# Kernel tuning notes

Measured on AMD Instinct MI355X. Metric: run time of the kernel, lower is better.

The kernel has to match this reference:

```python
import jax, jax.numpy as jnp
import numpy as np

B, S, IDIM, D, T, DUR_MAX = 32, 512, 256, 256, 4096, 16
EPS = 1e-6
SIGMA_C = 2.0
PAD = 0
LOG_SQRT_2PI = 0.9189385332046727  # 0.5*log(2*pi)


def setup_inputs() -> dict:
    rng = np.random.default_rng(0)
    # durations in [1, DUR_MAX); clip so each row's total length <= T (ragged tails)
    durs = rng.integers(1, DUR_MAX, size=(B, S))
    excl = np.cumsum(durs, axis=-1) - durs
    durs = np.minimum(durs, np.maximum(T - excl, 0))
    # token ids in [1, IDIM) so PAD=0 only appears via explicit padding
    text = rng.integers(1, IDIM, size=(B, S))
    embed = rng.standard_normal((IDIM, D)).astype(np.float32)
    embed[PAD] = 0.0  # padding_idx=0 row is zeros in nn.Embedding
    return {
        "text": jnp.asarray(text, dtype=jnp.int64),
        "durs": jnp.asarray(durs, dtype=jnp.int64),
        "embed": jnp.asarray(embed),
        "total_time": T,
    }


def reference(text, durs, embed, total_time):
    # F.pad(text/durs, [0, 2]) with value 0
    text_p = jnp.pad(text, ((0, 0), (0, 2)), constant_values=PAD)   # [B, S+2]
    durs_p = jnp.pad(durs, ((0, 0), (0, 2)), constant_values=0)     # [B, S+2]
    S2 = text_p.shape[-1]

    cum = jnp.cumsum(durs_p, axis=-1)                               # [B, S+2]
    durs_f = durs_p.astype(jnp.float32)
    # token centers: durs/2 + exclusive cumsum
    c = durs_f / 2.0 + (cum - durs_p).astype(jnp.float32)           # [B, S+2]
    sig = durs_f / SIGMA_C + EPS                                    # [B, S+2]

    t = jnp.arange(total_time, dtype=jnp.float32) + 0.5             # [T]
    z = (t[None, :, None] - c[:, None, :]) / sig[:, None, :]        # [B, T, S+2]
    # Normal(c, sig).log_prob(t).exp()
    w = jnp.exp(-0.5 * z * z - jnp.log(sig)[:, None, :] - LOG_SQRT_2PI)

    # zero weights on pad tokens, then normalize over tokens
    token_pad = (text_p == PAD)                                     # [B, S+2]
    w = jnp.where(token_pad[:, None, :], 0.0, w)
    w = w / (w.sum(-1, keepdims=True) + EPS)

    # frames beyond a row's total duration correspond to pad in `repeats`:
    # zero all weights there, then set the last token column to 1.0
    time_invalid = jnp.arange(total_time)[None, :] >= cum[:, -1:]   # [B, T]
    w = jnp.where(time_invalid[:, :, None], 0.0, w)
    last_col = (jnp.arange(S2) == S2 - 1)
    w = jnp.where(time_invalid[:, :, None] & last_col[None, None, :], 1.0, w)

    emb = embed[text_p]                                             # [B, S+2, D]
    return jnp.einsum("bts,bsd->btd", w, emb)                       # [B, T, D]
```

## Files before the change

kernel.cpp:

```cpp
#include <hip/hip_runtime.h>

#define B_ 32
#define S_ 512
#define D_ 256
#define T_ 4096
#define IDIM_ 256
#define EPS_ 1e-6f
#define INV_SQRT_2PI 0.3989422804014327f
#define NHALF_LOG2E -0.7213475204444817f
#define W_ 48

__global__ __launch_bounds__(512) void GaussianEmbedding_prep(
    const int* __restrict__ text, const int* __restrict__ durs,
    float4* __restrict__ toks, int* __restrict__ tof, int* __restrict__ totb)
{
    int b = blockIdx.x;
    int s = threadIdx.x;
    int dur = durs[b * S_ + s];
    int lane = s & 63, wv = s >> 6;

    int incl = dur;
    #pragma unroll
    for (int o = 1; o < 64; o <<= 1) {
        int v = __shfl_up(incl, o);
        if (lane >= o) incl += v;
    }
    __shared__ int wsum[8];
    if (lane == 63) wsum[wv] = incl;
    __syncthreads();
    int woff = 0;
    for (int i = 0; i < wv; ++i) woff += wsum[i];
    int excl = woff + incl - dur;

    if (s == 0) {
        int tot = 0;
        for (int i = 0; i < 8; ++i) tot += wsum[i];
        totb[b] = tot;
    }

    float df = (float)dur;
    float sig = df * 0.5f + EPS_;
    float inv = 1.0f / sig;
    float4 tk;
    tk.x = df * 0.5f + (float)excl;
    tk.y = inv;
    tk.z = INV_SQRT_2PI * inv;
    tk.w = __int_as_float(text[b * S_ + s] & (IDIM_ - 1));
    toks[b * S_ + s] = tk;

    for (int f = excl; f < excl + dur; ++f)
        tof[b * T_ + f] = s;
}

__global__ __launch_bounds__(256) void GaussianEmbedding_main(
    const float4* __restrict__ toks, const int* __restrict__ tof,
    const int* __restrict__ totb, const float* __restrict__ embed,
    float4* __restrict__ out)
{
    int wv = threadIdx.x >> 6;
    int lane = threadIdx.x & 63;
    int frame = __builtin_amdgcn_readfirstlane(blockIdx.x * 4 + wv);
    int b = frame >> 12;
    int t = frame & (T_ - 1);

    int total = totb[b];
    float4 acc = make_float4(0.f, 0.f, 0.f, 0.f);

    if (t < total) {
        int tlo = t - W_; if (tlo < 0) tlo = 0;
        int thi = t + W_; if (thi > total - 1) thi = total - 1;
        int lo = tof[b * T_ + tlo];
        int hi = tof[b * T_ + thi];

        float tc = (float)t + 0.5f;
        float psum = 0.f;
        for (int s = lo; s <= hi; ++s) {
            float4 tk = toks[b * S_ + s];
            float z = (tc - tk.x) * tk.y;
            float w = exp2f(NHALF_LOG2E * z * z) * tk.z;
            psum += w;
            int tok = __float_as_int(tk.w);
            float4 ev = ((const float4*)embed)[tok * (D_ / 4) + lane];
            acc.x += w * ev.x;
            acc.y += w * ev.y;
            acc.z += w * ev.z;
            acc.w += w * ev.w;
        }
        float invp = 1.0f / (psum + EPS_);
        acc.x *= invp; acc.y *= invp; acc.z *= invp; acc.w *= invp;
    }
    out[(size_t)frame * (D_ / 4) + lane] = acc;
}

extern "C" void kernel_launch(void* const* d_in, const int* in_sizes, int n_in,
                              void* d_out, int out_size, void* d_ws, size_t ws_size,
                              hipStream_t stream)
{
    const int* text    = (const int*)d_in[0];
    const int* durs    = (const int*)d_in[1];
    const float* embed = (const float*)d_in[2];

    float4* toks = (float4*)d_ws;
    int* tof  = (int*)((char*)d_ws + (size_t)B_ * S_ * sizeof(float4));
    int* totb = tof + (size_t)B_ * T_;

    GaussianEmbedding_prep<<<B_, S_, 0, stream>>>(text, durs, toks, tof, totb);
    GaussianEmbedding_main<<<(B_ * T_) / 4, 256, 0, stream>>>(
        toks, tof, totb, embed, (float4*)d_out);
}
```

Measured before the change: 183.3 us.

## Stage per-block token window in LDS, shrink window, use nontemporal stores

Each block of 4 frames now computes one shared token range, loads those token records into shared memory once, and has all four waves loop over the staged tokens. The window shrinks from 48 to 32 frames and is capped at 128 tokens. Output is written with nontemporal stores to avoid polluting cache, and the inner loop is unrolled by 4. The shared range is a union over four frames, so each wave evaluates a few extra negligible tokens, and two block-wide barriers are added; the narrower window slightly changes the approximation of the full-sequence normalization.

```diff
diff --git a/kernel.cpp b/kernel.cpp
--- a/kernel.cpp
+++ b/kernel.cpp
@@ -8,7 +8,10 @@
 #define EPS_ 1e-6f
 #define INV_SQRT_2PI 0.3989422804014327f
 #define NHALF_LOG2E -0.7213475204444817f
-#define W_ 48
+#define W_ 32
+#define NMAX_ 128
+
+typedef float float4n __attribute__((ext_vector_type(4)));
 
 __global__ __launch_bounds__(512) void GaussianEmbedding_prep(
     const int* __restrict__ text, const int* __restrict__ durs,
@@ -55,41 +58,61 @@
 __global__ __launch_bounds__(256) void GaussianEmbedding_main(
     const float4* __restrict__ toks, const int* __restrict__ tof,
     const int* __restrict__ totb, const float* __restrict__ embed,
-    float4* __restrict__ out)
+    float* __restrict__ out)
 {
     int wv = threadIdx.x >> 6;
     int lane = threadIdx.x & 63;
-    int frame = __builtin_amdgcn_readfirstlane(blockIdx.x * 4 + wv);
-    int b = frame >> 12;
-    int t = frame & (T_ - 1);
+    int blk = blockIdx.x;
+    int b  = blk >> 10;
+    int t0 = (blk & 1023) * 4;
 
     int total = totb[b];
-    float4 acc = make_float4(0.f, 0.f, 0.f, 0.f);
 
+    __shared__ float4 stoks[NMAX_];
+    __shared__ int shead[2];
+
+    if (threadIdx.x == 0) {
+        int lo = 0, n = 0;
+        if (t0 < total) {
+            int tlo = t0 - W_;      if (tlo < 0) tlo = 0;
+            int thi = t0 + 3 + W_;  if (thi > total - 1) thi = total - 1;
+            lo = tof[b * T_ + tlo];
+            int hi = tof[b * T_ + thi];
+            n = hi - lo + 1;
+            if (n > NMAX_) n = NMAX_;
+        }
+        shead[0] = lo; shead[1] = n;
+    }
+    __syncthreads();
+    int lo = shead[0], n = shead[1];
+    if (threadIdx.x < n)
+        stoks[threadIdx.x] = toks[b * S_ + lo + threadIdx.x];
+    __syncthreads();
+
+    int t = t0 + wv;
+    float4n acc = {0.f, 0.f, 0.f, 0.f};
     if (t < total) {
-        int tlo = t - W_; if (tlo < 0) tlo = 0;
-        int thi = t + W_; if (thi > total - 1) thi = total - 1;
-        int lo = tof[b * T_ + tlo];
-        int hi = tof[b * T_ + thi];
-
         float tc = (float)t + 0.5f;
         float psum = 0.f;
-        for (int s = lo; s <= hi; ++s) {
-            float4 tk = toks[b * S_ + s];
+        const float4* embed4 = (const float4*)embed;
+        #pragma unroll 4
+        for (int i = 0; i < n; ++i) {
+            float4 tk = stoks[i];
             float z = (tc - tk.x) * tk.y;
             float w = exp2f(NHALF_LOG2E * z * z) * tk.z;
             psum += w;
             int tok = __float_as_int(tk.w);
-            float4 ev = ((const float4*)embed)[tok * (D_ / 4) + lane];
+            float4 ev = embed4[tok * (D_ / 4) + lane];
             acc.x += w * ev.x;
             acc.y += w * ev.y;
             acc.z += w * ev.z;
             acc.w += w * ev.w;
         }
         float invp = 1.0f / (psum + EPS_);
-        acc.x *= invp; acc.y *= invp; acc.z *= invp; acc.w *= invp;
+        acc *= invp;
     }
-    out[(size_t)frame * (D_ / 4) + lane] = acc;
+    float4n* outv = (float4n*)out;
+    __builtin_nontemporal_store(acc, &outv[(size_t)(b * T_ + t) * (D_ / 4) + lane]);
 }
 
 extern "C" void kernel_launch(void* const* d_in, const int* in_sizes, int n_in,
@@ -106,5 +129,5 @@
 
     GaussianEmbedding_prep<<<B_, S_, 0, stream>>>(text, durs, toks, tof, totb);
     GaussianEmbedding_main<<<(B_ * T_) / 4, 256, 0, stream>>>(
-        toks, tof, totb, embed, (float4*)d_out);
+        toks, tof, totb, embed, (float*)d_out);
 }
```

Measured after the change: 174.1 us. 1.05x faster.

## Process four frames per wavefront to reuse token and embedding loads

Applied to the files above, without the earlier changes.

Each wavefront now computes four consecutive output frames, so every token record and embedding row it loads is shared across four accumulators instead of being reloaded per frame. The Gaussian window shrinks from 48 to 32 frames, and the prep kernel fills the tail of the frame-to-token map so index lookups past a row's total stay defined. Output is written with nontemporal stores. In exchange there are four times as many accumulator registers, fewer waves in flight, and a truncation window that is narrower and may drop more weight.

```diff
diff --git a/kernel.cpp b/kernel.cpp
--- a/kernel.cpp
+++ b/kernel.cpp
@@ -8,7 +8,9 @@
 #define EPS_ 1e-6f
 #define INV_SQRT_2PI 0.3989422804014327f
 #define NHALF_LOG2E -0.7213475204444817f
-#define W_ 48
+#define W_ 32
+
+typedef float float4n __attribute__((ext_vector_type(4)));
 
 __global__ __launch_bounds__(512) void GaussianEmbedding_prep(
     const int* __restrict__ text, const int* __restrict__ durs,
@@ -26,6 +28,7 @@
         if (lane >= o) incl += v;
     }
     __shared__ int wsum[8];
+    __shared__ int stot;
     if (lane == 63) wsum[wv] = incl;
     __syncthreads();
     int woff = 0;
@@ -36,7 +39,10 @@
         int tot = 0;
         for (int i = 0; i < 8; ++i) tot += wsum[i];
         totb[b] = tot;
+        stot = tot;
     }
+    __syncthreads();
+    int total = stot;
 
     float df = (float)dur;
     float sig = df * 0.5f + EPS_;
@@ -50,46 +56,63 @@
 
     for (int f = excl; f < excl + dur; ++f)
         tof[b * T_ + f] = s;
+    for (int f = total + s; f < T_; f += S_)
+        tof[b * T_ + f] = S_ - 1;
 }
 
 __global__ __launch_bounds__(256) void GaussianEmbedding_main(
-    const float4* __restrict__ toks, const int* __restrict__ tof,
-    const int* __restrict__ totb, const float* __restrict__ embed,
-    float4* __restrict__ out)
+    const float4n* __restrict__ toks, const int* __restrict__ tof,
+    const int* __restrict__ totb, const float4n* __restrict__ embed4,
+    float4n* __restrict__ out)
 {
-    int wv = threadIdx.x >> 6;
     int lane = threadIdx.x & 63;
-    int frame = __builtin_amdgcn_readfirstlane(blockIdx.x * 4 + wv);
-    int b = frame >> 12;
-    int t = frame & (T_ - 1);
+    int wave = __builtin_amdgcn_readfirstlane(blockIdx.x * 4 + (threadIdx.x >> 6));
+    int b  = wave >> 10;
+    int t0 = (wave & 1023) * 4;
 
     int total = totb[b];
-    float4 acc = make_float4(0.f, 0.f, 0.f, 0.f);
 
-    if (t < total) {
-        int tlo = t - W_; if (tlo < 0) tlo = 0;
-        int thi = t + W_; if (thi > total - 1) thi = total - 1;
+    float4n a0 = {0,0,0,0}, a1 = {0,0,0,0}, a2 = {0,0,0,0}, a3 = {0,0,0,0};
+
+    if (t0 < total) {
+        int tlo = t0 - W_;      if (tlo < 0) tlo = 0;
+        int thi = t0 + 3 + W_;  if (thi > total - 1) thi = total - 1;
         int lo = tof[b * T_ + tlo];
         int hi = tof[b * T_ + thi];
+        if (lo < 0) lo = 0; if (hi > S_ - 1) hi = S_ - 1; if (hi < lo) hi = lo;
+        lo = __builtin_amdgcn_readfirstlane(lo);
+        hi = __builtin_amdgcn_readfirstlane(hi);
 
-        float tc = (float)t + 0.5f;
-        float psum = 0.f;
+        float c0 = (float)t0 + 0.5f, c1 = c0 + 1.f, c2 = c0 + 2.f, c3 = c0 + 3.f;
+        float p0 = 0.f, p1 = 0.f, p2 = 0.f, p3 = 0.f;
+        #pragma unroll 2
         for (int s = lo; s <= hi; ++s) {
-            float4 tk = toks[b * S_ + s];
-            float z = (tc - tk.x) * tk.y;
-            float w = exp2f(NHALF_LOG2E * z * z) * tk.z;
-            psum += w;
+            float4n tk = toks[b * S_ + s];
             int tok = __float_as_int(tk.w);
-            float4 ev = ((const float4*)embed)[tok * (D_ / 4) + lane];
-            acc.x += w * ev.x;
-            acc.y += w * ev.y;
-            acc.z += w * ev.z;
-            acc.w += w * ev.w;
+            float4n ev = embed4[tok * (D_ / 4) + lane];
+            float z0 = (c0 - tk.x) * tk.y;
+            float z1 = (c1 - tk.x) * tk.y;
+            float z2 = (c2 - tk.x) * tk.y;
+            float z3 = (c3 - tk.x) * tk.y;
+            float w0 = exp2f(NHALF_LOG2E * z0 * z0) * tk.z;
+            float w1 = exp2f(NHALF_LOG2E * z1 * z1) * tk.z;
+            float w2 = exp2f(NHALF_LOG2E * z2 * z2) * tk.z;
+            float w3 = exp2f(NHALF_LOG2E * z3 * z3) * tk.z;
+            p0 += w0; p1 += w1; p2 += w2; p3 += w3;
+            a0 += w0 * ev; a1 += w1 * ev; a2 += w2 * ev; a3 += w3 * ev;
         }
-        float invp = 1.0f / (psum + EPS_);
-        acc.x *= invp; acc.y *= invp; acc.z *= invp; acc.w *= invp;
+        float s0 = (t0 + 0 < total) ? 1.0f / (p0 + EPS_) : 0.0f;
+        float s1 = (t0 + 1 < total) ? 1.0f / (p1 + EPS_) : 0.0f;
+        float s2 = (t0 + 2 < total) ? 1.0f / (p2 + EPS_) : 0.0f;
+        float s3 = (t0 + 3 < total) ? 1.0f / (p3 + EPS_) : 0.0f;
+        a0 *= s0; a1 *= s1; a2 *= s2; a3 *= s3;
     }
-    out[(size_t)frame * (D_ / 4) + lane] = acc;
+
+    size_t base = (size_t)(b * T_ + t0) * (D_ / 4) + lane;
+    __builtin_nontemporal_store(a0, out + base);
+    __builtin_nontemporal_store(a1, out + base + (D_ / 4));
+    __builtin_nontemporal_store(a2, out + base + 2 * (D_ / 4));
+    __builtin_nontemporal_store(a3, out + base + 3 * (D_ / 4));
 }
 
 extern "C" void kernel_launch(void* const* d_in, const int* in_sizes, int n_in,
@@ -105,6 +128,6 @@
     int* totb = tof + (size_t)B_ * T_;
 
     GaussianEmbedding_prep<<<B_, S_, 0, stream>>>(text, durs, toks, tof, totb);
-    GaussianEmbedding_main<<<(B_ * T_) / 4, 256, 0, stream>>>(
-        toks, tof, totb, embed, (float4*)d_out);
+    GaussianEmbedding_main<<<(B_ * T_) / 16, 256, 0, stream>>>(
+        (const float4n*)toks, tof, totb, (const float4n*)embed, (float4n*)d_out);
 }
```

Result: faster. 158.8 us (-13.3%).
